# Optimization experiments

Measured on AMD Instinct MI355X. Metric: run time of the kernel, lower is better.

Reference implementation:

```python
import jax, jax.numpy as jnp
import numpy as np

BETA = 100.0
H = 2048
W = 2048


def setup_inputs() -> dict:
    key = jax.random.key(0)
    heatmap = jax.random.normal(key, (1, 11, H, W), dtype=jnp.float32)
    return {"heatmap": heatmap}


def _soft_argmax(hm, xx, yy):
    # hm: (..., H, W); softmax over flattened H*W, then coordinate expectation
    flat = hm.reshape(hm.shape[:-2] + (hm.shape[-2] * hm.shape[-1],))
    sm = jax.nn.softmax(flat, axis=-1).reshape(hm.shape)
    ax = jnp.sum(sm * xx, axis=(-2, -1))
    ay = jnp.sum(sm * yy, axis=(-2, -1))
    return ax, ay


def reference(heatmap):
    b, n, h, w = heatmap.shape  # structurally b=1, n=11
    dt = heatmap.dtype
    hm = heatmap * jnp.asarray(BETA, dt)
    yy = jnp.broadcast_to(jnp.arange(h, dtype=dt)[:, None], (h, w))
    xx = jnp.broadcast_to(jnp.arange(w, dtype=dt)[None, :], (h, w))

    # init: channels 9,10 (last two), full-map soft-argmax
    ax, ay = _soft_argmax(hm[0, -2:], xx, yy)  # (2,), (2,)
    out = jnp.zeros((11, 2), dt)
    out = out.at[9:11, 0].set(ax).at[9:11, 1].set(ay)
    dis0 = out[10, 1] - out[9, 1]

    channels = hm[0, :9][::-1]  # iterate i = 8 .. 0
    idxs = jnp.arange(8, -1, -1)
    rows = jnp.arange(h, dtype=dt)[:, None]  # (H,1) row coordinates for band mask

    def body(carry, xs):
        out, dis, dis_sum, dis_num = carry
        i, ch = xs
        y_ip1 = jax.lax.dynamic_slice(out, (i + 1, 1), (1, 1))[0, 0]
        y_ip2 = jax.lax.dynamic_slice(out, (i + 2, 1), (1, 1))[0, 0]
        last_y = jnp.floor(y_ip1)            # emulates .long() (y >= 0)
        tmp_dis = jnp.ceil(y_ip2 - y_ip1)
        cond = jnp.abs(tmp_dis - dis) > 0.35 * dis
        dis_sum = jnp.where(cond, dis_sum + tmp_dis, dis_sum)
        dis_num = jnp.where(cond, dis_num + 1.0, dis_num)
        dis = jnp.where(cond, dis_sum / jnp.maximum(dis_num, 1.0), dis)
        start_raw = last_y - 1.8 * dis
        end_y = jnp.round(start_raw + 0.9 * 2.0 * dis)
        start_y = jnp.round(start_raw)
        mask = ((rows >= start_y) & (rows <= end_y)).astype(dt)  # (H,1)
        ax_i, ay_i = _soft_argmax(ch * mask, xx, yy)
        row = jnp.stack([ax_i, ay_i])[None, :]  # (1,2)
        out = jax.lax.dynamic_update_slice(out, row.astype(dt), (i, jnp.zeros((), idxs.dtype)))
        return (out, dis, dis_sum, dis_num), None

    zero = jnp.zeros((), dt)
    (out, _, _, _), _ = jax.lax.scan(body, (out, dis0, zero, zero), (idxs, channels))
    return out[None]  # (1, 11, 2)
```

## Files before the change

kernel.cpp:

```cpp
#include <hip/hip_runtime.h>
#include <math.h>

#define HH 2048
#define WW 2048
#define NB 256
#define STAGE_GRID 512


__device__ __forceinline__ float wave_fmax(float v) {
#pragma unroll
  for (int m = 1; m < 64; m <<= 1) v = fmaxf(v, __shfl_xor(v, m, 64));
  return v;
}
__device__ __forceinline__ float wave_fsum(float v) {
#pragma unroll
  for (int m = 1; m < 64; m <<= 1) v += __shfl_xor(v, m, 64);
  return v;
}

__device__ float block_fmax(float v) {
  __shared__ float s[4];
  v = wave_fmax(v);
  __syncthreads();
  if ((threadIdx.x & 63) == 0) s[threadIdx.x >> 6] = v;
  __syncthreads();
  return fmaxf(fmaxf(s[0], s[1]), fmaxf(s[2], s[3]));
}

__device__ void block_fsum3(float& a, float& b, float& c) {
  __shared__ float sa[4], sb[4], sc[4];
  a = wave_fsum(a); b = wave_fsum(b); c = wave_fsum(c);
  __syncthreads();
  if ((threadIdx.x & 63) == 0) {
    int w = threadIdx.x >> 6;
    sa[w] = a; sb[w] = b; sc[w] = c;
  }
  __syncthreads();
  a = (sa[0] + sa[1]) + (sa[2] + sa[3]);
  b = (sb[0] + sb[1]) + (sb[2] + sb[3]);
  c = (sc[0] + sc[1]) + (sc[2] + sc[3]);
}

__device__ float4 wave_row_partial(const float* __restrict__ rowp) {
  const int lane = threadIdx.x & 63;
  const float4* r4 = (const float4*)rowp;
  float d[32];
  float m = -INFINITY;
#pragma unroll
  for (int p = 0; p < 8; ++p) {
    float4 v = r4[lane + 64 * p];
    d[4 * p + 0] = v.x * 100.0f;
    d[4 * p + 1] = v.y * 100.0f;
    d[4 * p + 2] = v.z * 100.0f;
    d[4 * p + 3] = v.w * 100.0f;
    m = fmaxf(m, fmaxf(fmaxf(d[4 * p], d[4 * p + 1]), fmaxf(d[4 * p + 2], d[4 * p + 3])));
  }
  float M = wave_fmax(m);
  float z = 0.0f, sx = 0.0f;
#pragma unroll
  for (int p = 0; p < 8; ++p) {
    float c0 = (float)(4 * (lane + 64 * p));
#pragma unroll
    for (int k = 0; k < 4; ++k) {
      float e = expf(d[4 * p + k] - M);
      z += e;
      sx += e * (c0 + (float)k);
    }
  }
  z = wave_fsum(z);
  sx = wave_fsum(sx);
  return make_float4(M, z, sx, 0.0f);
}

__device__ void merge_partials(const float4* __restrict__ arr, int s, int e,
                               float& M, float& Z, float& SX, float& SY) {
  float m = -INFINITY;
  for (int r = s + (int)threadIdx.x; r <= e; r += NB) m = fmaxf(m, arr[r].x);
  M = block_fmax(m);
  float z = 0.0f, sx = 0.0f, sy = 0.0f;
  for (int r = s + (int)threadIdx.x; r <= e; r += NB) {
    float4 p = arr[r];
    float w = expf(p.x - M);
    z  += w * p.y;
    sx += w * p.z;
    sy += w * p.y * (float)r;
  }
  block_fsum3(z, sx, sy);
  Z = z; SX = sx; SY = sy;
}

__device__ void finalize2(float M, float Z, float SX, float SY, int s, int e,
                          bool valid, float& ax, float& ay) {
  int nin = valid ? (e - s + 1) : 0;
  int nout = HH - nin;
  if (nout > 0) {
    float M2 = fmaxf(M, 0.0f);
    float wi = (M == M2) ? 1.0f : expf(M - M2);
    float wo = (M2 == 0.0f) ? 1.0f : expf(-M2);
    Z *= wi; SX *= wi; SY *= wi;
    float nout_e = (float)nout * (float)WW;
    float sox = (float)nout * 2096128.0f;
    float sinr = valid ? (float)(((long)(s + e) * (e - s + 1)) / 2) : 0.0f;
    float soy = (2096128.0f - sinr) * 2048.0f;
    Z  += wo * nout_e;
    SX += wo * sox;
    SY += wo * soy;
  }
  ax = SX / Z;
  ay = SY / Z;
}


__global__ __launch_bounds__(NB) void k_rows910(const float* __restrict__ heat,
                                                float* ws) {
  float4* F = (float4*)(ws + 512);
  int gw = blockIdx.x * 4 + (threadIdx.x >> 6);
  int ch = 9 + (gw >> 11);
  int r = gw & (HH - 1);
  float4 t = wave_row_partial(heat + ((size_t)ch * HH + r) * WW);
  if ((threadIdx.x & 63) == 0) F[gw] = t;
}

__global__ __launch_bounds__(NB) void k_stage(const float* __restrict__ heat,
                                              float* ws, float* __restrict__ out,
                                              int i) {
  float4* F  = (float4*)(ws + 512);
  float4* B0 = F + 4096;
  float4* B1 = B0 + HH;

  float st[28];
  if (i == 8) {
    for (int k = 0; k < 28; ++k) st[k] = 0.0f;
    float M, Z, SX, SY, ax, ay;
    merge_partials(F, 0, HH - 1, M, Z, SX, SY);
    finalize2(M, Z, SX, SY, 0, HH - 1, true, ax, ay);
    st[18] = ax; st[19] = ay;
    merge_partials(F + HH, 0, HH - 1, M, Z, SX, SY);
    finalize2(M, Z, SX, SY, 0, HH - 1, true, ax, ay);
    st[20] = ax; st[21] = ay;
    st[22] = st[21] - st[19];
    st[23] = 0.0f; st[24] = 0.0f;
  } else {
    const float* prev = ws + 32 * (i + 1);
    for (int k = 0; k < 28; ++k) st[k] = prev[k];
    const int j = i + 1;
    const float4* Bprev = (j & 1) ? B1 : B0;
    int s = (int)st[25], e = (int)st[26];
    bool valid = (st[27] != 0.0f);
    float M = -INFINITY, Z = 0.0f, SX = 0.0f, SY = 0.0f, ax, ay;
    if (valid) merge_partials(Bprev, s, e, M, Z, SX, SY);
    finalize2(M, Z, SX, SY, s, e, valid, ax, ay);
    st[2 * j] = ax; st[2 * j + 1] = ay;
  }

  if (i >= 0) {
    float y1 = st[2 * (i + 1) + 1];
    float y2 = st[2 * (i + 2) + 1];
    float dis = st[22], dsum = st[23], dnum = st[24];
    float last_y = floorf(y1);
    float tmp = ceilf(y2 - y1);
    bool cond = fabsf(tmp - dis) > 0.35f * dis;
    if (cond) { dsum += tmp; dnum += 1.0f; dis = dsum / fmaxf(dnum, 1.0f); }
    float start_raw = last_y - 1.8f * dis;
    float end_f   = rintf(start_raw + 1.8f * dis);
    float start_f = rintf(start_raw);
    int s2 = (int)fmaxf(start_f, 0.0f);
    int e2 = (int)fminf(end_f, (float)(HH - 1));
    bool bvalid = (s2 <= e2) && (end_f >= 0.0f) && (start_f <= (float)(HH - 1));
    st[22] = dis; st[23] = dsum; st[24] = dnum;
    st[25] = (float)s2; st[26] = (float)e2; st[27] = bvalid ? 1.0f : 0.0f;

    float4* Bcur = (i & 1) ? B1 : B0;
    if (bvalid) {
      const int wid = (int)(blockIdx.x * 4) + (threadIdx.x >> 6);
      for (int r = s2 + wid; r <= e2; r += (int)gridDim.x * 4) {
        float4 t = wave_row_partial(heat + ((size_t)i * HH + r) * WW);
        if ((threadIdx.x & 63) == 0) Bcur[r] = t;
      }
    }
    if (blockIdx.x == 0 && threadIdx.x == 0) {
      float* slot = ws + 32 * i;
      for (int k = 0; k < 28; ++k) slot[k] = st[k];
    }
  } else {
    if (blockIdx.x == 0 && threadIdx.x < 22) out[threadIdx.x] = st[threadIdx.x];
  }
}

extern "C" void kernel_launch(void* const* d_in, const int* in_sizes, int n_in,
                              void* d_out, int out_size, void* d_ws, size_t ws_size,
                              hipStream_t stream) {
  const float* heat = (const float*)d_in[0];
  float* out = (float*)d_out;
  float* ws = (float*)d_ws;
  hipLaunchKernelGGL(k_rows910, dim3(1024), dim3(NB), 0, stream, heat, ws);
  for (int i = 8; i >= 0; --i) {
    hipLaunchKernelGGL(k_stage, dim3(STAGE_GRID), dim3(NB), 0, stream, heat, ws, out, i);
  }
  hipLaunchKernelGGL(k_stage, dim3(1), dim3(NB), 0, stream, heat, ws, out, -1);
}
```

Baseline: 243.5 us.

## Precompute all row partials in one pass, run dependent chain in single block

Instead of nine serial stage launches that each compute row partials only for the banded rows of one channel, one wide kernel now computes per-row softmax partials for all 11 channels up front. A single 1024-thread block then walks the dependent chain, merging the precomputed partials over each band. This turns eleven launches into two and removes the serial dependency between heavy stages. The cost is reading the full 11-channel heatmap rather than only the band rows, and running the sequential merges in a single block.

```diff
diff --git a/kernel.cpp b/kernel.cpp
--- a/kernel.cpp
+++ b/kernel.cpp
@@ -3,9 +3,11 @@
 
 #define HH 2048
 #define WW 2048
+#define NROWS (11 * HH)
 #define NB 256
-#define STAGE_GRID 512
-
+#define SGRID 1024
+#define NBC 1024
+#define NWC (NBC / 64)
 
 __device__ __forceinline__ float wave_fmax(float v) {
 #pragma unroll
@@ -16,29 +18,6 @@
 #pragma unroll
   for (int m = 1; m < 64; m <<= 1) v += __shfl_xor(v, m, 64);
   return v;
-}
-
-__device__ float block_fmax(float v) {
-  __shared__ float s[4];
-  v = wave_fmax(v);
-  __syncthreads();
-  if ((threadIdx.x & 63) == 0) s[threadIdx.x >> 6] = v;
-  __syncthreads();
-  return fmaxf(fmaxf(s[0], s[1]), fmaxf(s[2], s[3]));
-}
-
-__device__ void block_fsum3(float& a, float& b, float& c) {
-  __shared__ float sa[4], sb[4], sc[4];
-  a = wave_fsum(a); b = wave_fsum(b); c = wave_fsum(c);
-  __syncthreads();
-  if ((threadIdx.x & 63) == 0) {
-    int w = threadIdx.x >> 6;
-    sa[w] = a; sb[w] = b; sc[w] = c;
-  }
-  __syncthreads();
-  a = (sa[0] + sa[1]) + (sa[2] + sa[3]);
-  b = (sb[0] + sb[1]) + (sb[2] + sb[3]);
-  c = (sc[0] + sc[1]) + (sc[2] + sc[3]);
 }
 
 __device__ float4 wave_row_partial(const float* __restrict__ rowp) {
@@ -72,20 +51,46 @@
   return make_float4(M, z, sx, 0.0f);
 }
 
+__device__ float blockc_fmax(float v) {
+  __shared__ float s[NWC];
+  v = wave_fmax(v);
+  __syncthreads();
+  if ((threadIdx.x & 63) == 0) s[threadIdx.x >> 6] = v;
+  __syncthreads();
+  float r = s[0];
+#pragma unroll
+  for (int k = 1; k < NWC; ++k) r = fmaxf(r, s[k]);
+  return r;
+}
+__device__ void blockc_fsum3(float& a, float& b, float& c) {
+  __shared__ float sa[NWC], sb[NWC], sc[NWC];
+  a = wave_fsum(a); b = wave_fsum(b); c = wave_fsum(c);
+  __syncthreads();
+  if ((threadIdx.x & 63) == 0) {
+    int w = threadIdx.x >> 6;
+    sa[w] = a; sb[w] = b; sc[w] = c;
+  }
+  __syncthreads();
+  float ra = 0.0f, rb = 0.0f, rc = 0.0f;
+#pragma unroll
+  for (int k = 0; k < NWC; ++k) { ra += sa[k]; rb += sb[k]; rc += sc[k]; }
+  a = ra; b = rb; c = rc;
+}
+
 __device__ void merge_partials(const float4* __restrict__ arr, int s, int e,
                                float& M, float& Z, float& SX, float& SY) {
   float m = -INFINITY;
-  for (int r = s + (int)threadIdx.x; r <= e; r += NB) m = fmaxf(m, arr[r].x);
-  M = block_fmax(m);
+  for (int r = s + (int)threadIdx.x; r <= e; r += NBC) m = fmaxf(m, arr[r].x);
+  M = blockc_fmax(m);
   float z = 0.0f, sx = 0.0f, sy = 0.0f;
-  for (int r = s + (int)threadIdx.x; r <= e; r += NB) {
+  for (int r = s + (int)threadIdx.x; r <= e; r += NBC) {
     float4 p = arr[r];
     float w = expf(p.x - M);
     z  += w * p.y;
     sx += w * p.z;
     sy += w * p.y * (float)r;
   }
-  block_fsum3(z, sx, sy);
+  blockc_fsum3(z, sx, sy);
   Z = z; SX = sx; SY = sy;
 }
 
@@ -111,52 +116,33 @@
 }
 
 
-__global__ __launch_bounds__(NB) void k_rows910(const float* __restrict__ heat,
-                                                float* ws) {
+__global__ __launch_bounds__(NB) void k_rows_all(const float* __restrict__ heat,
+                                                 float* ws) {
   float4* F = (float4*)(ws + 512);
-  int gw = blockIdx.x * 4 + (threadIdx.x >> 6);
-  int ch = 9 + (gw >> 11);
-  int r = gw & (HH - 1);
-  float4 t = wave_row_partial(heat + ((size_t)ch * HH + r) * WW);
-  if ((threadIdx.x & 63) == 0) F[gw] = t;
+  const int nw = SGRID * (NB / 64);
+  for (int r = blockIdx.x * (NB / 64) + ((int)threadIdx.x >> 6); r < NROWS; r += nw) {
+    float4 t = wave_row_partial(heat + (size_t)r * WW);
+    if ((threadIdx.x & 63) == 0) F[r] = t;
+  }
 }
 
-__global__ __launch_bounds__(NB) void k_stage(const float* __restrict__ heat,
-                                              float* ws, float* __restrict__ out,
-                                              int i) {
-  float4* F  = (float4*)(ws + 512);
-  float4* B0 = F + 4096;
-  float4* B1 = B0 + HH;
+__global__ __launch_bounds__(NBC) void k_chain(float* ws, float* __restrict__ out) {
+  const float4* F = (const float4*)(ws + 512);
+  float st[22];
+  float M, Z, SX, SY, ax, ay;
 
-  float st[28];
-  if (i == 8) {
-    for (int k = 0; k < 28; ++k) st[k] = 0.0f;
-    float M, Z, SX, SY, ax, ay;
-    merge_partials(F, 0, HH - 1, M, Z, SX, SY);
-    finalize2(M, Z, SX, SY, 0, HH - 1, true, ax, ay);
-    st[18] = ax; st[19] = ay;
-    merge_partials(F + HH, 0, HH - 1, M, Z, SX, SY);
-    finalize2(M, Z, SX, SY, 0, HH - 1, true, ax, ay);
-    st[20] = ax; st[21] = ay;
-    st[22] = st[21] - st[19];
-    st[23] = 0.0f; st[24] = 0.0f;
-  } else {
-    const float* prev = ws + 32 * (i + 1);
-    for (int k = 0; k < 28; ++k) st[k] = prev[k];
-    const int j = i + 1;
-    const float4* Bprev = (j & 1) ? B1 : B0;
-    int s = (int)st[25], e = (int)st[26];
-    bool valid = (st[27] != 0.0f);
-    float M = -INFINITY, Z = 0.0f, SX = 0.0f, SY = 0.0f, ax, ay;
-    if (valid) merge_partials(Bprev, s, e, M, Z, SX, SY);
-    finalize2(M, Z, SX, SY, s, e, valid, ax, ay);
-    st[2 * j] = ax; st[2 * j + 1] = ay;
-  }
+  merge_partials(F + 9 * HH, 0, HH - 1, M, Z, SX, SY);
+  finalize2(M, Z, SX, SY, 0, HH - 1, true, ax, ay);
+  st[18] = ax; st[19] = ay;
+  merge_partials(F + 10 * HH, 0, HH - 1, M, Z, SX, SY);
+  finalize2(M, Z, SX, SY, 0, HH - 1, true, ax, ay);
+  st[20] = ax; st[21] = ay;
 
-  if (i >= 0) {
+  float dis = st[21] - st[19], dsum = 0.0f, dnum = 0.0f;
+
+  for (int i = 8; i >= 0; --i) {
     float y1 = st[2 * (i + 1) + 1];
     float y2 = st[2 * (i + 2) + 1];
-    float dis = st[22], dsum = st[23], dnum = st[24];
     float last_y = floorf(y1);
     float tmp = ceilf(y2 - y1);
     bool cond = fabsf(tmp - dis) > 0.35f * dis;
@@ -164,27 +150,16 @@
     float start_raw = last_y - 1.8f * dis;
     float end_f   = rintf(start_raw + 1.8f * dis);
     float start_f = rintf(start_raw);
-    int s2 = (int)fmaxf(start_f, 0.0f);
-    int e2 = (int)fminf(end_f, (float)(HH - 1));
-    bool bvalid = (s2 <= e2) && (end_f >= 0.0f) && (start_f <= (float)(HH - 1));
-    st[22] = dis; st[23] = dsum; st[24] = dnum;
-    st[25] = (float)s2; st[26] = (float)e2; st[27] = bvalid ? 1.0f : 0.0f;
+    int s = (int)fmaxf(start_f, 0.0f);
+    int e = (int)fminf(end_f, (float)(HH - 1));
+    bool valid = (s <= e) && (end_f >= 0.0f) && (start_f <= (float)(HH - 1));
+    M = -INFINITY; Z = 0.0f; SX = 0.0f; SY = 0.0f;
+    if (valid) merge_partials(F + (size_t)i * HH, s, e, M, Z, SX, SY);
+    finalize2(M, Z, SX, SY, s, e, valid, ax, ay);
+    st[2 * i] = ax; st[2 * i + 1] = ay;
+  }
 
-    float4* Bcur = (i & 1) ? B1 : B0;
-    if (bvalid) {
-      const int wid = (int)(blockIdx.x * 4) + (threadIdx.x >> 6);
-      for (int r = s2 + wid; r <= e2; r += (int)gridDim.x * 4) {
-        float4 t = wave_row_partial(heat + ((size_t)i * HH + r) * WW);
-        if ((threadIdx.x & 63) == 0) Bcur[r] = t;
-      }
-    }
-    if (blockIdx.x == 0 && threadIdx.x == 0) {
-      float* slot = ws + 32 * i;
-      for (int k = 0; k < 28; ++k) slot[k] = st[k];
-    }
-  } else {
-    if (blockIdx.x == 0 && threadIdx.x < 22) out[threadIdx.x] = st[threadIdx.x];
-  }
+  if (threadIdx.x < 22) out[threadIdx.x] = st[threadIdx.x];
 }
 
 extern "C" void kernel_launch(void* const* d_in, const int* in_sizes, int n_in,
@@ -193,9 +168,6 @@
   const float* heat = (const float*)d_in[0];
   float* out = (float*)d_out;
   float* ws = (float*)d_ws;
-  hipLaunchKernelGGL(k_rows910, dim3(1024), dim3(NB), 0, stream, heat, ws);
-  for (int i = 8; i >= 0; --i) {
-    hipLaunchKernelGGL(k_stage, dim3(STAGE_GRID), dim3(NB), 0, stream, heat, ws, out, i);
-  }
-  hipLaunchKernelGGL(k_stage, dim3(1), dim3(NB), 0, stream, heat, ws, out, -1);
+  hipLaunchKernelGGL(k_rows_all, dim3(SGRID), dim3(NB), 0, stream, heat, ws);
+  hipLaunchKernelGGL(k_chain, dim3(1), dim3(NBC), 0, stream, ws, out);
 }
```

Measured after the change: 267.1 us. 9.7% more time.

## Fuse all stages into one persistent kernel with atomic grid barriers

Applied to the files above, without the earlier changes.

Replaces the eleven sequential kernel launches with a single persistent kernel of 256 blocks. Block 0 acts as leader: it merges partials and computes each band window, then publishes it through an atomic packet. The worker blocks poll for that packet and compute row partials for the band, then check in through hierarchical atomic counters. This removes per-launch overhead and inter-kernel gaps at the cost of spin-wait synchronisation. It also uses fewer waves per stage, and block 0 does no row work during stages.

```diff
diff --git a/kernel.cpp b/kernel.cpp
--- a/kernel.cpp
+++ b/kernel.cpp
@@ -1,10 +1,14 @@
 #include <hip/hip_runtime.h>
 #include <math.h>
+#include <stdint.h>
 
 #define HH 2048
 #define WW 2048
 #define NB 256
-#define STAGE_GRID 512
+#define GRID 256
+#define NWAVES (GRID * 4)
+#define NWW 1020
+#define CTRL_INTS 2048
 
 
 __device__ __forceinline__ float wave_fmax(float v) {
@@ -16,29 +20,6 @@
 #pragma unroll
   for (int m = 1; m < 64; m <<= 1) v += __shfl_xor(v, m, 64);
   return v;
-}
-
-__device__ float block_fmax(float v) {
-  __shared__ float s[4];
-  v = wave_fmax(v);
-  __syncthreads();
-  if ((threadIdx.x & 63) == 0) s[threadIdx.x >> 6] = v;
-  __syncthreads();
-  return fmaxf(fmaxf(s[0], s[1]), fmaxf(s[2], s[3]));
-}
-
-__device__ void block_fsum3(float& a, float& b, float& c) {
-  __shared__ float sa[4], sb[4], sc[4];
-  a = wave_fsum(a); b = wave_fsum(b); c = wave_fsum(c);
-  __syncthreads();
-  if ((threadIdx.x & 63) == 0) {
-    int w = threadIdx.x >> 6;
-    sa[w] = a; sb[w] = b; sc[w] = c;
-  }
-  __syncthreads();
-  a = (sa[0] + sa[1]) + (sa[2] + sa[3]);
-  b = (sb[0] + sb[1]) + (sb[2] + sb[3]);
-  c = (sc[0] + sc[1]) + (sc[2] + sc[3]);
 }
 
 __device__ float4 wave_row_partial(const float* __restrict__ rowp) {
@@ -70,6 +51,28 @@
   z = wave_fsum(z);
   sx = wave_fsum(sx);
   return make_float4(M, z, sx, 0.0f);
+}
+
+__device__ float block_fmax(float v) {
+  __shared__ float s[4];
+  v = wave_fmax(v);
+  __syncthreads();
+  if ((threadIdx.x & 63) == 0) s[threadIdx.x >> 6] = v;
+  __syncthreads();
+  return fmaxf(fmaxf(s[0], s[1]), fmaxf(s[2], s[3]));
+}
+__device__ void block_fsum3(float& a, float& b, float& c) {
+  __shared__ float sa[4], sb[4], sc[4];
+  a = wave_fsum(a); b = wave_fsum(b); c = wave_fsum(c);
+  __syncthreads();
+  if ((threadIdx.x & 63) == 0) {
+    int w = threadIdx.x >> 6;
+    sa[w] = a; sb[w] = b; sc[w] = c;
+  }
+  __syncthreads();
+  a = (sa[0] + sa[1]) + (sa[2] + sa[3]);
+  b = (sb[0] + sb[1]) + (sb[2] + sb[3]);
+  c = (sc[0] + sc[1]) + (sc[2] + sc[3]);
 }
 
 __device__ void merge_partials(const float4* __restrict__ arr, int s, int e,
@@ -110,80 +113,115 @@
   ay = SY / Z;
 }
 
-
-__global__ __launch_bounds__(NB) void k_rows910(const float* __restrict__ heat,
-                                                float* ws) {
-  float4* F = (float4*)(ws + 512);
-  int gw = blockIdx.x * 4 + (threadIdx.x >> 6);
-  int ch = 9 + (gw >> 11);
-  int r = gw & (HH - 1);
-  float4 t = wave_row_partial(heat + ((size_t)ch * HH + r) * WW);
-  if ((threadIdx.x & 63) == 0) F[gw] = t;
-}
-
-__global__ __launch_bounds__(NB) void k_stage(const float* __restrict__ heat,
-                                              float* ws, float* __restrict__ out,
-                                              int i) {
-  float4* F  = (float4*)(ws + 512);
+__device__ void checkin(int* ctrl, int st) {
+  __syncthreads();
+  if (threadIdx.x == 0) {
+    __threadfence();
+    int g = (int)blockIdx.x & 7;
+    int old = atomicAdd(ctrl + 16 + st * 128 + g * 16, 1);
+    if (old == 31) atomicAdd(ctrl + 16 + 1280 + st * 16, 32);
+  }
+}
+
+__device__ void leader_wait(int* ctrl, int st) {
+  if (threadIdx.x == 0) {
+    while (__hip_atomic_load(ctrl + 16 + 1280 + st * 16, __ATOMIC_ACQUIRE,
+                             __HIP_MEMORY_SCOPE_AGENT) < GRID)
+      __builtin_amdgcn_s_sleep(1);
+    __threadfence();
+  }
+  __syncthreads();
+}
+
+__global__ __launch_bounds__(NB) void k_fused(const float* __restrict__ heat,
+                                              float* ws, float* __restrict__ out) {
+  int* ctrl = (int*)ws;
+  uint64_t* ep = (uint64_t*)ws;
+  float4* F  = (float4*)(ws + CTRL_INTS);
   float4* B0 = F + 4096;
   float4* B1 = B0 + HH;
-
-  float st[28];
-  if (i == 8) {
-    for (int k = 0; k < 28; ++k) st[k] = 0.0f;
+  const int tid = (int)threadIdx.x;
+  const int wv  = tid >> 6;
+
+  {
+    const int wid = (int)blockIdx.x * 4 + wv;
+    for (int rr = wid; rr < 2 * HH; rr += NWAVES) {
+      int ch = 9 + (rr >> 11), r = rr & (HH - 1);
+      float4 t = wave_row_partial(heat + ((size_t)ch * HH + r) * WW);
+      if ((tid & 63) == 0) F[rr] = t;
+    }
+  }
+  checkin(ctrl, 9);
+
+  if (blockIdx.x == 0) {
+    __shared__ float s_out[22];
+    leader_wait(ctrl, 9);
     float M, Z, SX, SY, ax, ay;
     merge_partials(F, 0, HH - 1, M, Z, SX, SY);
     finalize2(M, Z, SX, SY, 0, HH - 1, true, ax, ay);
-    st[18] = ax; st[19] = ay;
+    float ax9 = ax, ay9 = ay;
     merge_partials(F + HH, 0, HH - 1, M, Z, SX, SY);
     finalize2(M, Z, SX, SY, 0, HH - 1, true, ax, ay);
-    st[20] = ax; st[21] = ay;
-    st[22] = st[21] - st[19];
-    st[23] = 0.0f; st[24] = 0.0f;
+    if (tid == 0) { s_out[18] = ax9; s_out[19] = ay9; s_out[20] = ax; s_out[21] = ay; }
+
+    float y1 = ay9, y2 = ay;
+    float dis = ay - ay9, dsum = 0.0f, dnum = 0.0f;
+
+    for (int i = 8; i >= 0; --i) {
+      float last_y = floorf(y1);
+      float tmp = ceilf(y2 - y1);
+      bool cond = fabsf(tmp - dis) > 0.35f * dis;
+      if (cond) { dsum += tmp; dnum += 1.0f; dis = dsum / fmaxf(dnum, 1.0f); }
+      float start_raw = last_y - 1.8f * dis;
+      float end_f   = rintf(start_raw + 1.8f * dis);
+      float start_f = rintf(start_raw);
+      int s2 = (int)fmaxf(start_f, 0.0f);
+      int e2 = (int)fminf(end_f, (float)(HH - 1));
+      bool bvalid = (s2 <= e2) && (end_f >= 0.0f) && (start_f <= (float)(HH - 1));
+
+      if (tid == 0) {
+        uint64_t pkt = ((uint64_t)(100 + i) << 40) | ((uint64_t)(uint32_t)e2 << 20)
+                     | ((uint64_t)(uint32_t)s2 << 4) | (bvalid ? 2u : 0u);
+        __hip_atomic_store(ep, pkt, __ATOMIC_RELEASE, __HIP_MEMORY_SCOPE_AGENT);
+      }
+      checkin(ctrl, i);
+      leader_wait(ctrl, i);
+
+      M = -INFINITY; Z = 0.0f; SX = 0.0f; SY = 0.0f;
+      const float4* Bc = (i & 1) ? B1 : B0;
+      if (bvalid) merge_partials(Bc, s2, e2, M, Z, SX, SY);
+      finalize2(M, Z, SX, SY, s2, e2, bvalid, ax, ay);
+      if (tid == 0) { s_out[2 * i] = ax; s_out[2 * i + 1] = ay; }
+      y2 = y1; y1 = ay;
+    }
+    __syncthreads();
+    if (tid < 22) out[tid] = s_out[tid];
   } else {
-    const float* prev = ws + 32 * (i + 1);
-    for (int k = 0; k < 28; ++k) st[k] = prev[k];
-    const int j = i + 1;
-    const float4* Bprev = (j & 1) ? B1 : B0;
-    int s = (int)st[25], e = (int)st[26];
-    bool valid = (st[27] != 0.0f);
-    float M = -INFINITY, Z = 0.0f, SX = 0.0f, SY = 0.0f, ax, ay;
-    if (valid) merge_partials(Bprev, s, e, M, Z, SX, SY);
-    finalize2(M, Z, SX, SY, s, e, valid, ax, ay);
-    st[2 * j] = ax; st[2 * j + 1] = ay;
-  }
-
-  if (i >= 0) {
-    float y1 = st[2 * (i + 1) + 1];
-    float y2 = st[2 * (i + 2) + 1];
-    float dis = st[22], dsum = st[23], dnum = st[24];
-    float last_y = floorf(y1);
-    float tmp = ceilf(y2 - y1);
-    bool cond = fabsf(tmp - dis) > 0.35f * dis;
-    if (cond) { dsum += tmp; dnum += 1.0f; dis = dsum / fmaxf(dnum, 1.0f); }
-    float start_raw = last_y - 1.8f * dis;
-    float end_f   = rintf(start_raw + 1.8f * dis);
-    float start_f = rintf(start_raw);
-    int s2 = (int)fmaxf(start_f, 0.0f);
-    int e2 = (int)fminf(end_f, (float)(HH - 1));
-    bool bvalid = (s2 <= e2) && (end_f >= 0.0f) && (start_f <= (float)(HH - 1));
-    st[22] = dis; st[23] = dsum; st[24] = dnum;
-    st[25] = (float)s2; st[26] = (float)e2; st[27] = bvalid ? 1.0f : 0.0f;
-
-    float4* Bcur = (i & 1) ? B1 : B0;
-    if (bvalid) {
-      const int wid = (int)(blockIdx.x * 4) + (threadIdx.x >> 6);
-      for (int r = s2 + wid; r <= e2; r += (int)gridDim.x * 4) {
-        float4 t = wave_row_partial(heat + ((size_t)i * HH + r) * WW);
-        if ((threadIdx.x & 63) == 0) Bcur[r] = t;
+    __shared__ uint64_t sp;
+    const int wid = ((int)blockIdx.x - 1) * 4 + wv;
+    for (int k = 8; k >= 0; --k) {
+      if (tid == 0) {
+        uint64_t p;
+        while (((p = __hip_atomic_load(ep, __ATOMIC_ACQUIRE,
+                                       __HIP_MEMORY_SCOPE_AGENT)) >> 40)
+               != (uint64_t)(100 + k))
+          __builtin_amdgcn_s_sleep(1);
+        sp = p;
       }
-    }
-    if (blockIdx.x == 0 && threadIdx.x == 0) {
-      float* slot = ws + 32 * i;
-      for (int k = 0; k < 28; ++k) slot[k] = st[k];
-    }
-  } else {
-    if (blockIdx.x == 0 && threadIdx.x < 22) out[threadIdx.x] = st[threadIdx.x];
+      __syncthreads();
+      uint64_t p = sp;
+      bool valid = (p & 2u) != 0;
+      int s2 = (int)((p >> 4)  & 0xFFFF);
+      int e2 = (int)((p >> 20) & 0xFFFF);
+      float4* Bcur = (k & 1) ? B1 : B0;
+      if (valid) {
+        for (int r = s2 + wid; r <= e2; r += NWW) {
+          float4 t = wave_row_partial(heat + ((size_t)k * HH + r) * WW);
+          if ((tid & 63) == 0) Bcur[r] = t;
+        }
+      }
+      checkin(ctrl, k);
+    }
   }
 }
 
@@ -193,9 +231,6 @@
   const float* heat = (const float*)d_in[0];
   float* out = (float*)d_out;
   float* ws = (float*)d_ws;
-  hipLaunchKernelGGL(k_rows910, dim3(1024), dim3(NB), 0, stream, heat, ws);
-  for (int i = 8; i >= 0; --i) {
-    hipLaunchKernelGGL(k_stage, dim3(STAGE_GRID), dim3(NB), 0, stream, heat, ws, out, i);
-  }
-  hipLaunchKernelGGL(k_stage, dim3(1), dim3(NB), 0, stream, heat, ws, out, -1);
-}
+  hipMemsetAsync(d_ws, 0, CTRL_INTS * sizeof(int), stream);
+  hipLaunchKernelGGL(k_fused, dim3(GRID), dim3(NB), 0, stream, heat, ws, out);
+}
```

New measurement: 436.3 us. +79.2%, slower.
